# Performance work log

Hardware: AMD Instinct MI355X
Metric: run time of the kernel (lower is better)

The kernel has to match this reference:

```python
import jax, jax.numpy as jnp
import numpy as np

B, S, CACHE, HID, NH, NKV, HD, INTER = 2, 1024, 2048, 2048, 8, 1, 256, 16384
EPS = 1e-6
SOFTCAP = 50.0
SCALE = HD ** -0.5  # query_pre_attn_scalar is None -> head_dim**-0.5
NEG = -1e9


def _rms(x, w, eps=EPS):
    # Gemma RMSNorm: fp32 norm, output scaled by (1 + weight)
    x32 = x.astype(jnp.float32)
    n = x32 * jax.lax.rsqrt(jnp.mean(x32 * x32, axis=-1, keepdims=True) + eps)
    return (n * (1.0 + w)).astype(x.dtype)


def _rope(x, cos, sin):
    # half-split complex rotation (Gemma apply_rotary_emb): first half real, second half imag
    d2 = x.shape[-1] // 2
    x1, x2 = x[..., :d2], x[..., d2:]
    c = cos[None, :, None, :]
    s = sin[None, :, None, :]
    return jnp.concatenate([x1 * c - x2 * s, x1 * s + x2 * c], axis=-1).astype(x.dtype)


def setup_inputs() -> dict:
    key = jax.random.key(0)
    ks = jax.random.split(key, 8)
    sc = lambda k, sh, f: jax.random.normal(k, sh, jnp.float32) * f
    inp = {}
    inp["hidden_states"] = sc(ks[0], (B, S, HID), 1.0)
    inv = 1.0 / (10000.0 ** (np.arange(0, HD, 2, dtype=np.float32) / HD))
    t = np.arange(S, dtype=np.float32)[:, None] * inv[None, :]
    inp["cos"] = jnp.asarray(np.cos(t), jnp.float32)
    inp["sin"] = jnp.asarray(np.sin(t), jnp.float32)
    inp["kv_write_indices"] = jnp.arange(S, dtype=jnp.int32)
    inp["k_cache"] = jnp.zeros((B, CACHE, NKV, HD), jnp.float32)
    inp["v_cache"] = jnp.zeros((B, CACHE, NKV, HD), jnp.float32)
    i = jnp.arange(S)[:, None]
    j = jnp.arange(CACHE)[None, :]
    inp["mask"] = jnp.where(j <= i, 0.0, NEG).astype(jnp.float32)[None, None]  # [1,1,S,CACHE]
    inp["w_qkv"] = sc(ks[1], ((NH + 2 * NKV) * HD, HID), 0.02)
    inp["w_o"] = sc(ks[2], (HID, NH * HD), 0.02)
    inp["w_gate"] = sc(ks[3], (INTER, HID), 0.02)
    inp["w_up"] = sc(ks[4], (INTER, HID), 0.02)
    inp["w_down"] = sc(ks[5], (HID, INTER), 0.02)
    inp["ln_in"] = jnp.zeros((HID,), jnp.float32)
    inp["ln_post"] = jnp.zeros((HID,), jnp.float32)
    inp["q_norm"] = jnp.zeros((HD,), jnp.float32)
    inp["k_norm"] = jnp.zeros((HD,), jnp.float32)
    return inp


def reference(hidden_states, cos, sin, kv_write_indices, k_cache, v_cache, mask,
              w_qkv, w_o, w_gate, w_up, w_down, ln_in, ln_post, q_norm, k_norm):
    # ---- attention sub-block ----
    res = hidden_states
    x = _rms(hidden_states, ln_in)
    qkv = x @ w_qkv.T  # [B,S,(NH+2*NKV)*HD]
    xq, xk, xv = jnp.split(qkv, [NH * HD, NH * HD + NKV * HD], axis=-1)
    xq = xq.reshape(B, S, NH, HD)
    xk = xk.reshape(B, S, NKV, HD)
    xv = xv.reshape(B, S, NKV, HD)
    xq = _rms(xq, q_norm)  # QK-norm
    xk = _rms(xk, k_norm)
    xq = _rope(xq, cos, sin)
    xk = _rope(xk, cos, sin)
    # KV-cache write (index_copy_ on dim 1)
    k_cache = k_cache.at[:, kv_write_indices].set(xk)
    v_cache = v_cache.at[:, kv_write_indices].set(xv)
    key = jnp.repeat(k_cache, NH // NKV, axis=2)  # [B,CACHE,NH,HD]
    val = jnp.repeat(v_cache, NH // NKV, axis=2)
    scores = jnp.einsum('bshd,bthd->bhst', xq * SCALE, key)  # [B,NH,S,CACHE]
    scores = jnp.tanh(scores / SOFTCAP) * SOFTCAP            # logit softcapping
    probs = jax.nn.softmax(scores + mask, axis=-1)
    out = jnp.einsum('bhst,bthd->bshd', probs, val).reshape(B, S, NH * HD)
    h = res + out @ w_o.T
    # ---- MLP sub-block ----
    res = h
    x = _rms(h, ln_post)
    gate = jax.nn.gelu(x @ w_gate.T, approximate=True)
    up = x @ w_up.T
    return res + (gate * up) @ w_down.T
```

## Files before the change

### kernel.cpp

```cpp
#include <hip/hip_runtime.h>
#include <hip/hip_bf16.h>

typedef __attribute__((ext_vector_type(8))) short short8;
typedef __attribute__((ext_vector_type(4))) float f32x4;
typedef unsigned short u16;

#define B_N 2
#define S_N 1024
#define HID_N 2048
#define NH_N 8
#define HD_N 256
#define INTER_N 16384

#define GLB(p) ((const __attribute__((address_space(1))) void*)(p))
#define AS3(p) ((__attribute__((address_space(3))) void*)(p))

__device__ inline u16 f2b_rn(float f) {
    union { float f; unsigned int u; } x; x.f = f;
    unsigned int r = x.u + 0x7fffu + ((x.u >> 16) & 1u);
    return (u16)(r >> 16);
}
__device__ inline float b2f(u16 h) {
    union { unsigned int u; float f; } x; x.u = ((unsigned int)h) << 16;
    return x.f;
}
__device__ inline float gelu_fast(float v) {
    float z = 0.7978845608028654f * (v + 0.044715f * v * v * v);
    float e = exp2f(z * 2.8853900817779268f);
    float th = 1.f - 2.f * __builtin_amdgcn_rcpf(e + 1.f);
    return 0.5f * v * (1.f + th);
}

__global__ __launch_bounds__(256) void convert_f2b(const float* __restrict__ in,
                                                   u16* __restrict__ out, int n4) {
    int i = blockIdx.x * 256 + threadIdx.x;
    int stride = gridDim.x * 256;
    for (; i < n4; i += stride) {
        float4 v = reinterpret_cast<const float4*>(in)[i];
        u16 o[4] = { f2b_rn(v.x), f2b_rn(v.y), f2b_rn(v.z), f2b_rn(v.w) };
        reinterpret_cast<ulonglong1*>(out)[i] = *reinterpret_cast<ulonglong1*>(o);
    }
}

__global__ __launch_bounds__(256) void convert_gu(const float* __restrict__ wg,
                                                  const float* __restrict__ wu,
                                                  u16* __restrict__ out, int n4) {
    int i = blockIdx.x * 256 + threadIdx.x;
    int stride = gridDim.x * 256;
    for (; i < n4; i += stride) {
        const int e = i << 2;
        const int r = e >> 11, c = e & 2047;
        const int rg = ((r >> 5) << 6) + (r & 31);
        float4 g = reinterpret_cast<const float4*>(wg)[i];
        u16 og[4] = { f2b_rn(g.x), f2b_rn(g.y), f2b_rn(g.z), f2b_rn(g.w) };
        *reinterpret_cast<ulonglong1*>(out + (size_t)rg * 2048 + c) =
            *reinterpret_cast<ulonglong1*>(og);
        float4 u = reinterpret_cast<const float4*>(wu)[i];
        u16 ou[4] = { f2b_rn(u.x), f2b_rn(u.y), f2b_rn(u.z), f2b_rn(u.w) };
        *reinterpret_cast<ulonglong1*>(out + (size_t)(rg + 32) * 2048 + c) =
            *reinterpret_cast<ulonglong1*>(ou);
    }
}

__global__ __launch_bounds__(256) void rmsnorm_k(const float* __restrict__ x,
                                                 const float* __restrict__ w,
                                                 u16* __restrict__ out) {
    const int row = blockIdx.x;
    const int tid = threadIdx.x;
    const float* xr = x + (size_t)row * HID_N;
    const float4* xr4 = reinterpret_cast<const float4*>(xr);
    float4 a = xr4[tid * 2], b = xr4[tid * 2 + 1];
    float s = a.x*a.x + a.y*a.y + a.z*a.z + a.w*a.w
            + b.x*b.x + b.y*b.y + b.z*b.z + b.w*b.w;
    for (int off = 32; off > 0; off >>= 1) s += __shfl_xor(s, off, 64);
    __shared__ float red[4];
    if ((tid & 63) == 0) red[tid >> 6] = s;
    __syncthreads();
    float tot = red[0] + red[1] + red[2] + red[3];
    float inv = rsqrtf(tot * (1.0f / HID_N) + 1e-6f);
    const float4* w4 = reinterpret_cast<const float4*>(w);
    float4 wa = w4[tid * 2], wb = w4[tid * 2 + 1];
    short8 o;
    o[0] = (short)f2b_rn(a.x * inv * (1.f + wa.x));
    o[1] = (short)f2b_rn(a.y * inv * (1.f + wa.y));
    o[2] = (short)f2b_rn(a.z * inv * (1.f + wa.z));
    o[3] = (short)f2b_rn(a.w * inv * (1.f + wa.w));
    o[4] = (short)f2b_rn(b.x * inv * (1.f + wb.x));
    o[5] = (short)f2b_rn(b.y * inv * (1.f + wb.y));
    o[6] = (short)f2b_rn(b.z * inv * (1.f + wb.z));
    o[7] = (short)f2b_rn(b.w * inv * (1.f + wb.w));
    reinterpret_cast<short8*>(out + (size_t)row * HID_N)[tid] = o;
}

__global__ __launch_bounds__(256) void qkv_post_k(const float* __restrict__ qkv,
                                                  const float* __restrict__ cosb,
                                                  const float* __restrict__ sinb,
                                                  const int* __restrict__ kvw,
                                                  const float* __restrict__ qn,
                                                  const float* __restrict__ kn,
                                                  u16* __restrict__ qb,
                                                  u16* __restrict__ kb,
                                                  u16* __restrict__ vt) {
    const int bs = blockIdx.x, vi = blockIdx.y;
    const int b = bs >> 10, s = bs & 1023;
    const int tid = threadIdx.x;
    const float* row = qkv + (size_t)bs * 2560;
    const int sdst = kvw[s];
    if (vi == 9) {
        vt[((size_t)(b * 256 + tid)) * 1024 + sdst] = f2b_rn(row[2304 + tid]);
        return;
    }
    __shared__ float buf[256];
    __shared__ float red[4];
    float val = row[vi * 256 + tid];
    float ss = val * val;
    for (int off = 32; off > 0; off >>= 1) ss += __shfl_xor(ss, off, 64);
    if ((tid & 63) == 0) red[tid >> 6] = ss;
    __syncthreads();
    float ms = (red[0] + red[1] + red[2] + red[3]) * (1.f / 256.f) + 1e-6f;
    const float* nw = (vi < 8) ? qn : kn;
    float nrm = val * rsqrtf(ms) * (1.f + nw[tid]);
    buf[tid] = nrm;
    __syncthreads();
    const float cv = cosb[s * 128 + (tid & 127)];
    const float sv = sinb[s * 128 + (tid & 127)];
    float o;
    if (tid < 128) o = buf[tid] * cv - buf[tid + 128] * sv;
    else           o = buf[tid - 128] * sv + buf[tid] * cv;
    if (vi < 8) qb[(((size_t)(b * 8 + vi)) * 1024 + s) * 256 + tid] = f2b_rn(o * 0.0625f);
    else        kb[((size_t)(b * 1024 + sdst)) * 256 + tid] = f2b_rn(o);
}

__global__ __launch_bounds__(256) void attn_k(const u16* __restrict__ qb,
                                              const u16* __restrict__ kb,
                                              const u16* __restrict__ vt,
                                              float* __restrict__ po,
                                              float* __restrict__ pl) {
    const int qt = blockIdx.x;
    const int h  = blockIdx.y;
    const int c  = blockIdx.z >> 1;
    const int b  = blockIdx.z & 1;
    if (qt < 4 * c) return;
    const int tid = threadIdx.x, lane = tid & 63, wid = tid >> 6;
    const int g = lane >> 4, li = lane & 15;
    const int q0 = qt * 64 + wid * 16;
    const int kv_lo = c * 256;
    __shared__ u16 pbuf[4][16 * 32];

    short8 qf[8];
    const size_t qbase = (((size_t)(b * 8 + h)) * 1024 + q0 + li) * 256;
    #pragma unroll
    for (int kk = 0; kk < 8; ++kk)
        qf[kk] = *reinterpret_cast<const short8*>(qb + qbase + kk * 32 + g * 8);

    f32x4 o[16], o1;
    #pragma unroll
    for (int d = 0; d < 16; ++d) o[d] = f32x4{0.f, 0.f, 0.f, 0.f};
    o1 = f32x4{0.f, 0.f, 0.f, 0.f};
    short8 onesf;
    #pragma unroll
    for (int j = 0; j < 8; ++j) onesf[j] = (short)0x3F80;

    const int nt = (min(kv_lo + 256, q0 + 16) - kv_lo + 31) >> 5;
    const int prd = li * 32 + ((g * 8) ^ (((li >> 2) & 3) * 8));

    for (int t = 0; t < nt; ++t) {
        const int kv0 = kv_lo + t * 32;
        f32x4 sc[2];
        sc[0] = f32x4{0.f, 0.f, 0.f, 0.f};
        sc[1] = f32x4{0.f, 0.f, 0.f, 0.f};
        #pragma unroll
        for (int ch = 0; ch < 2; ++ch) {
            const size_t kbase = ((size_t)(b * 1024 + kv0 + ch * 16 + li)) * 256;
            #pragma unroll
            for (int kk = 0; kk < 8; ++kk) {
                short8 kf = *reinterpret_cast<const short8*>(kb + kbase + kk * 32 + g * 8);
                sc[ch] = __builtin_amdgcn_mfma_f32_16x16x32_bf16(qf[kk], kf, sc[ch], 0, 0, 0);
            }
        }
        #pragma unroll
        for (int reg = 0; reg < 4; ++reg) {
            const int qrow = q0 + g * 4 + reg;
            const int prow = g * 4 + reg;
            const int pswz = ((prow >> 2) & 3) * 8;
            #pragma unroll
            for (int ch = 0; ch < 2; ++ch) {
                const int col = kv0 + ch * 16 + li;
                float s = sc[ch][reg];
                float e = exp2f(s * 0.05770780163555854f);
                float th = 1.f - 2.f * __builtin_amdgcn_rcpf(e + 1.f);
                float pv = exp2f(th * 72.13475204444817f);
                pv = (col <= qrow) ? pv : 0.f;
                pbuf[wid][prow * 32 + ((ch * 16 + li) ^ pswz)] = f2b_rn(pv);
            }
        }
        short8 pf = *reinterpret_cast<const short8*>(&pbuf[wid][prd]);
        o1 = __builtin_amdgcn_mfma_f32_16x16x32_bf16(pf, onesf, o1, 0, 0, 0);
        #pragma unroll
        for (int dth = 0; dth < 2; ++dth) {
            short8 vf[8];
            #pragma unroll
            for (int d8 = 0; d8 < 8; ++d8) {
                const int dt = dth * 8 + d8;
                vf[d8] = *reinterpret_cast<const short8*>(
                    vt + ((size_t)(b * 256 + dt * 16 + li)) * 1024 + kv0 + g * 8);
            }
            #pragma unroll
            for (int d8 = 0; d8 < 8; ++d8)
                o[dth * 8 + d8] = __builtin_amdgcn_mfma_f32_16x16x32_bf16(pf, vf[d8], o[dth * 8 + d8], 0, 0, 0);
        }
    }
    const size_t pbase = ((size_t)((c * 2 + b) * 8 + h)) * 1024;
    #pragma unroll
    for (int reg = 0; reg < 4; ++reg) {
        const int row = q0 + g * 4 + reg;
        #pragma unroll
        for (int dt = 0; dt < 16; ++dt)
            po[(pbase + row) * 256 + dt * 16 + li] = o[dt][reg];
        if (li == 0) pl[pbase + row] = o1[reg];
    }
}

__global__ __launch_bounds__(256) void attn_red_k(const float* __restrict__ po,
                                                  const float* __restrict__ pl,
                                                  u16* __restrict__ out) {
    const int gid = blockIdx.x;
    const int b = gid >> 10, s = gid & 1023;
    const int tid = threadIdx.x;
    const int h = tid >> 5, d0 = (tid & 31) * 8;
    const int cmax = s >> 8;
    float l = 0.f;
    float4 a0 = float4{0.f, 0.f, 0.f, 0.f}, a1 = float4{0.f, 0.f, 0.f, 0.f};
    for (int ci = 0; ci <= cmax; ++ci) {
        const size_t r = ((size_t)((ci * 2 + b) * 8 + h)) * 1024 + s;
        l += pl[r];
        float4 b0 = *reinterpret_cast<const float4*>(po + r * 256 + d0);
        float4 b1 = *reinterpret_cast<const float4*>(po + r * 256 + d0 + 4);
        a0.x += b0.x; a0.y += b0.y; a0.z += b0.z; a0.w += b0.w;
        a1.x += b1.x; a1.y += b1.y; a1.z += b1.z; a1.w += b1.w;
    }
    const float inv = 1.f / l;
    u16 r[8] = { f2b_rn(a0.x * inv), f2b_rn(a0.y * inv), f2b_rn(a0.z * inv), f2b_rn(a0.w * inv),
                 f2b_rn(a1.x * inv), f2b_rn(a1.y * inv), f2b_rn(a1.z * inv), f2b_rn(a1.w * inv) };
    *reinterpret_cast<ulonglong2*>(out + ((size_t)gid) * 2048 + h * 256 + d0) =
        *reinterpret_cast<ulonglong2*>(r);
}

template <int EPI>
__global__ __launch_bounds__(256) void gemm_bt(const u16* __restrict__ A,
                                               const u16* __restrict__ W,
                                               const float* __restrict__ res,
                                               float* __restrict__ outf,
                                               int M, int N, int K) {
    __shared__ u16 As[2][128 * 64];
    __shared__ u16 Bs[2][128 * 64];
    const int tid = threadIdx.x, lane = tid & 63, wid = tid >> 6;
    const int g = lane >> 4, li = lane & 15;
    const int wr = wid >> 1, wc = wid & 1;
    const int m0 = blockIdx.x * 128, n0 = blockIdx.y * 128;

    f32x4 acc[4][4];
    #pragma unroll
    for (int m = 0; m < 4; ++m)
        #pragma unroll
        for (int n = 0; n < 4; ++n) acc[m][n] = f32x4{0.f, 0.f, 0.f, 0.f};

    const int lrow = lane >> 3;
    const int lcol = (lane & 7) ^ lrow;
    const u16* ga0 = A + (size_t)(m0 + wid * 32 + lrow) * K + lcol * 8;
    const u16* gb0 = W + (size_t)(n0 + wid * 32 + lrow) * K + lcol * 8;
    const int lbase = wid * 32 * 64;

    auto STAGE = [&](int buf, int k0) {
        #pragma unroll
        for (int i = 0; i < 4; ++i) {
            __builtin_amdgcn_global_load_lds(GLB(ga0 + k0 + (size_t)(i * 8) * K),
                                             AS3(&As[buf][lbase + i * 8 * 64]), 16, 0, 0);
            __builtin_amdgcn_global_load_lds(GLB(gb0 + k0 + (size_t)(i * 8) * K),
                                             AS3(&Bs[buf][lbase + i * 8 * 64]), 16, 0, 0);
        }
    };

    const int NT = K >> 6;
    STAGE(0, 0);
    int cur = 0;
    for (int t = 0; t < NT; ++t) {
        if (t + 1 < NT) {
            STAGE(cur ^ 1, (t + 1) << 6);
            asm volatile("s_waitcnt vmcnt(8)" ::: "memory");
        } else {
            asm volatile("s_waitcnt vmcnt(0)" ::: "memory");
        }
        __builtin_amdgcn_s_barrier();
        __builtin_amdgcn_sched_barrier(0);
        #pragma unroll
        for (int kh = 0; kh < 2; ++kh) {
            short8 af[4], bfr[4];
            #pragma unroll
            for (int m = 0; m < 4; ++m) {
                int rw = wr * 64 + m * 16 + li;
                int slot = (kh * 4 + g) ^ (rw & 7);
                af[m] = *reinterpret_cast<const short8*>(&As[cur][rw * 64 + slot * 8]);
            }
            #pragma unroll
            for (int n = 0; n < 4; ++n) {
                int rw = wc * 64 + n * 16 + li;
                int slot = (kh * 4 + g) ^ (rw & 7);
                bfr[n] = *reinterpret_cast<const short8*>(&Bs[cur][rw * 64 + slot * 8]);
            }
            #pragma unroll
            for (int m = 0; m < 4; ++m)
                #pragma unroll
                for (int n = 0; n < 4; ++n)
                    acc[m][n] = __builtin_amdgcn_mfma_f32_16x16x32_bf16(af[m], bfr[n], acc[m][n], 0, 0, 0);
        }
        __builtin_amdgcn_s_barrier();
        cur ^= 1;
    }

    #pragma unroll
    for (int m = 0; m < 4; ++m) {
        #pragma unroll
        for (int n = 0; n < 4; ++n) {
            #pragma unroll
            for (int reg = 0; reg < 4; ++reg) {
                int row = m0 + wr * 64 + m * 16 + g * 4 + reg;
                int col = n0 + wc * 64 + n * 16 + li;
                size_t idx = (size_t)row * N + col;
                float v = acc[m][n][reg];
                if (EPI == 0) outf[idx] = v;
                else          outf[idx] = v + res[idx];
            }
        }
    }
}

template <int EPI>
__global__ __launch_bounds__(1024) void gemm256(const u16* __restrict__ A,
                                                const u16* __restrict__ W,
                                                float* __restrict__ outf,
                                                u16* __restrict__ outb,
                                                int M, int N, int K, int kcN) {
    __shared__ u16 Als[2][256 * 64];
    __shared__ u16 Bls[2][256 * 64];
    const int tid = threadIdx.x, lane = tid & 63, wid = tid >> 6;
    const int g = lane >> 4, li = lane & 15;
    const int wm = wid >> 2, wn = wid & 3;
    const int m0 = blockIdx.y * 256, n0 = blockIdx.x * 256;

    int koff = 0, Keff = K;
    if (EPI == 4) {
        Keff = K / kcN;
        koff = blockIdx.z * Keff;
        outf += (size_t)blockIdx.z * M * N;
    }

    f32x4 acc[4][4];
    #pragma unroll
    for (int m = 0; m < 4; ++m)
        #pragma unroll
        for (int n = 0; n < 4; ++n) acc[m][n] = f32x4{0.f, 0.f, 0.f, 0.f};

    const int trow = tid >> 3;
    const int sgr = ((tid & 7) ^ (trow & 7)) * 8;
    const u16* Asrc = A + (size_t)(m0 + trow) * K + koff + sgr;
    const u16* Bsrc = W + (size_t)(n0 + trow) * K + koff + sgr;
    const int dstb = wid * 512;

    auto STAGE = [&](int bf, int kt) {
        const int k0 = kt << 6;
        #pragma unroll
        for (int i = 0; i < 2; ++i) {
            __builtin_amdgcn_global_load_lds(GLB(Asrc + (size_t)(i * 128) * K + k0),
                                             AS3(&Als[bf][i * 8192 + dstb]), 16, 0, 0);
            __builtin_amdgcn_global_load_lds(GLB(Bsrc + (size_t)(i * 128) * K + k0),
                                             AS3(&Bls[bf][i * 8192 + dstb]), 16, 0, 0);
        }
    };

    const int NT = Keff >> 6;
    STAGE(0, 0);
    int cur = 0;
    for (int t = 0; t < NT; ++t) {
        if (t + 1 < NT) {
            STAGE(cur ^ 1, t + 1);
            asm volatile("s_waitcnt vmcnt(4)" ::: "memory");
        } else {
            asm volatile("s_waitcnt vmcnt(0)" ::: "memory");
        }
        __builtin_amdgcn_s_barrier();
        __builtin_amdgcn_sched_barrier(0);
        #pragma unroll
        for (int kh = 0; kh < 2; ++kh) {
            short8 af[4], bfr[4];
            #pragma unroll
            for (int m = 0; m < 4; ++m) {
                const int rw = wm * 64 + m * 16 + li;
                const int slot = (kh * 4 + g) ^ (rw & 7);
                af[m] = *reinterpret_cast<const short8*>(&Als[cur][rw * 64 + slot * 8]);
            }
            #pragma unroll
            for (int n = 0; n < 4; ++n) {
                const int rw = wn * 64 + n * 16 + li;
                const int slot = (kh * 4 + g) ^ (rw & 7);
                bfr[n] = *reinterpret_cast<const short8*>(&Bls[cur][rw * 64 + slot * 8]);
            }
            #pragma unroll
            for (int m = 0; m < 4; ++m)
                #pragma unroll
                for (int n = 0; n < 4; ++n)
                    acc[m][n] = __builtin_amdgcn_mfma_f32_16x16x32_bf16(af[m], bfr[n], acc[m][n], 0, 0, 0);
        }
        __builtin_amdgcn_s_barrier();
        cur ^= 1;
    }

    if (EPI == 5) {
        #pragma unroll
        for (int m = 0; m < 4; ++m) {
            #pragma unroll
            for (int n = 0; n < 2; ++n) {
                const int col = (n0 >> 1) + wn * 32 + n * 16 + li;
                #pragma unroll
                for (int reg = 0; reg < 4; ++reg) {
                    const int row = m0 + wm * 64 + m * 16 + g * 4 + reg;
                    float gt = gelu_fast(acc[m][n][reg]);
                    float up = acc[m][n + 2][reg];
                    outb[(size_t)row * INTER_N + col] = f2b_rn(gt * up);
                }
            }
        }
    } else {
        #pragma unroll
        for (int m = 0; m < 4; ++m) {
            #pragma unroll
            for (int n = 0; n < 4; ++n) {
                #pragma unroll
                for (int reg = 0; reg < 4; ++reg) {
                    const int row = m0 + wm * 64 + m * 16 + g * 4 + reg;
                    const int col = n0 + wn * 64 + n * 16 + li;
                    outf[(size_t)row * N + col] = acc[m][n][reg];
                }
            }
        }
    }
}

__global__ __launch_bounds__(256) void reduce4_k(const float* __restrict__ part,
                                                 const float* __restrict__ res,
                                                 float* __restrict__ out, int n4) {
    int i = blockIdx.x * 256 + threadIdx.x;
    int stride = gridDim.x * 256;
    const size_t ps = (size_t)HID_N * B_N * S_N / 4;
    const float4* p4 = reinterpret_cast<const float4*>(part);
    const float4* r4 = reinterpret_cast<const float4*>(res);
    float4* o4 = reinterpret_cast<float4*>(out);
    for (; i < n4; i += stride) {
        float4 a = p4[i], b = p4[i + ps], c = p4[i + 2 * ps], d = p4[i + 3 * ps];
        float4 r = r4[i];
        float4 o;
        o.x = r.x + a.x + b.x + c.x + d.x;
        o.y = r.y + a.y + b.y + c.y + d.y;
        o.z = r.z + a.z + b.z + c.z + d.z;
        o.w = r.w + a.w + b.w + c.w + d.w;
        o4[i] = o;
    }
}

extern "C" void kernel_launch(void* const* d_in, const int* in_sizes, int n_in,
                              void* d_out, int out_size, void* d_ws, size_t ws_size,
                              hipStream_t stream) {
    (void)in_sizes; (void)n_in; (void)out_size; (void)ws_size;
    const float* hs     = (const float*)d_in[0];
    const float* cosb   = (const float*)d_in[1];
    const float* sinb   = (const float*)d_in[2];
    const int*   kvw    = (const int*)d_in[3];
    const float* wqkv   = (const float*)d_in[7];
    const float* wo     = (const float*)d_in[8];
    const float* wg     = (const float*)d_in[9];
    const float* wu     = (const float*)d_in[10];
    const float* wd     = (const float*)d_in[11];
    const float* ln_in  = (const float*)d_in[12];
    const float* ln_post= (const float*)d_in[13];
    const float* qn     = (const float*)d_in[14];
    const float* kn     = (const float*)d_in[15];
    float* out = (float*)d_out;

    char* p = (char*)d_ws;
    auto alloc = [&](size_t bytes) {
        char* r = p;
        p += (bytes + 255) & ~(size_t)255;
        return r;
    };
    u16* wqkv_b = (u16*)alloc(2560ull * 2048 * 2);
    u16* wo_b   = (u16*)alloc(2048ull * 2048 * 2);
    u16* wgu_b  = (u16*)alloc(32768ull * 2048 * 2);
    u16* wd_b   = (u16*)alloc(2048ull * 16384 * 2);
    u16* xn     = (u16*)alloc(2048ull * 2048 * 2);
    float* qkvf = (float*)alloc(2048ull * 2560 * 4);
    u16* qbuf   = (u16*)alloc(2ull * 8 * 1024 * 256 * 2);
    u16* kbuf   = (u16*)alloc(2ull * 1024 * 256 * 2);
    u16* vtbuf  = (u16*)alloc(2ull * 256 * 1024 * 2);
    u16* attn_o = (u16*)alloc(2048ull * 2048 * 2);
    float* hbuf = (float*)alloc(2048ull * 2048 * 4);
    u16* x2     = (u16*)alloc(2048ull * 2048 * 2);
    u16* actb   = (u16*)alloc(2048ull * 16384 * 2);
    float* po   = (float*)alloc(8ull * 8 * 1024 * 256 * 4);
    float* plse = (float*)alloc(8ull * 8 * 1024 * 4);
    float* partials = (float*)d_ws;

    auto conv = [&](const float* src, u16* dst, long n) {
        int n4 = (int)(n / 4);
        long blk = (n4 + 255) / 256;
        if (blk > 4096) blk = 4096;
        convert_f2b<<<dim3((unsigned)blk), dim3(256), 0, stream>>>(src, dst, n4);
    };
    conv(wqkv, wqkv_b, 2560l * 2048);
    conv(wo,   wo_b,   2048l * 2048);
    convert_gu<<<dim3(4096), dim3(256), 0, stream>>>(wg, wu, wgu_b, 8388608);
    conv(wd,   wd_b,   2048l * 16384);

    rmsnorm_k<<<dim3(2048), dim3(256), 0, stream>>>(hs, ln_in, xn);
    gemm_bt<0><<<dim3(16, 20), dim3(256), 0, stream>>>(xn, wqkv_b, nullptr,
                                                       qkvf, 2048, 2560, 2048);
    qkv_post_k<<<dim3(2048, 10), dim3(256), 0, stream>>>(qkvf, cosb, sinb, kvw, qn, kn,
                                                         qbuf, kbuf, vtbuf);
    attn_k<<<dim3(16, 8, 8), dim3(256), 0, stream>>>(qbuf, kbuf, vtbuf, po, plse);
    attn_red_k<<<dim3(2048), dim3(256), 0, stream>>>(po, plse, attn_o);
    gemm_bt<1><<<dim3(16, 16), dim3(256), 0, stream>>>(attn_o, wo_b, hs,
                                                       hbuf, 2048, 2048, 2048);
    rmsnorm_k<<<dim3(2048), dim3(256), 0, stream>>>(hbuf, ln_post, x2);
    gemm256<5><<<dim3(128, 8), dim3(1024), 0, stream>>>(x2, wgu_b, nullptr, actb,
                                                        2048, 16384, 2048, 1);
    gemm256<4><<<dim3(8, 8, 4), dim3(1024), 0, stream>>>(actb, wd_b, partials, nullptr,
                                                         2048, 2048, 16384, 4);
    reduce4_k<<<dim3(2048), dim3(256), 0, stream>>>(partials, hbuf, out, 1048576);
}
```

Measured before the change: 811.2 us.

## Replace GEMM kernels with unified 128x128 tile, 16-wave GEMM

Both the 4-wave 128x128 gemm_bt and the 16-wave 256x256 gemm256 are replaced by a single 16-wave kernel using 128x128 tiles, where each wave owns a 32x32 sub-tile. The gate/up weight interleave is changed from 32-row to 16-row groups to match the new per-wave column split. The aim is more waves per tile to hide latency and a larger grid for the big MLP GEMMs. In exchange, the arithmetic intensity per wave and the data reuse per tile drop, which raises LDS and global traffic per FLOP on the large GEMMs.

Measured after the change: 900.3 us. +11.0%, slower.

```diff
diff --git a/kernel.cpp b/kernel.cpp
--- a/kernel.cpp
+++ b/kernel.cpp
@@ -50,14 +50,14 @@
     for (; i < n4; i += stride) {
         const int e = i << 2;
         const int r = e >> 11, c = e & 2047;
-        const int rg = ((r >> 5) << 6) + (r & 31);
+        const int rg = ((r >> 4) << 5) + (r & 15);
         float4 g = reinterpret_cast<const float4*>(wg)[i];
         u16 og[4] = { f2b_rn(g.x), f2b_rn(g.y), f2b_rn(g.z), f2b_rn(g.w) };
         *reinterpret_cast<ulonglong1*>(out + (size_t)rg * 2048 + c) =
             *reinterpret_cast<ulonglong1*>(og);
         float4 u = reinterpret_cast<const float4*>(wu)[i];
         u16 ou[4] = { f2b_rn(u.x), f2b_rn(u.y), f2b_rn(u.z), f2b_rn(u.w) };
-        *reinterpret_cast<ulonglong1*>(out + (size_t)(rg + 32) * 2048 + c) =
+        *reinterpret_cast<ulonglong1*>(out + (size_t)(rg + 16) * 2048 + c) =
             *reinterpret_cast<ulonglong1*>(ou);
     }
 }
@@ -247,106 +247,18 @@
 }
 
 template <int EPI>
-__global__ __launch_bounds__(256) void gemm_bt(const u16* __restrict__ A,
-                                               const u16* __restrict__ W,
-                                               const float* __restrict__ res,
-                                               float* __restrict__ outf,
-                                               int M, int N, int K) {
-    __shared__ u16 As[2][128 * 64];
-    __shared__ u16 Bs[2][128 * 64];
-    const int tid = threadIdx.x, lane = tid & 63, wid = tid >> 6;
-    const int g = lane >> 4, li = lane & 15;
-    const int wr = wid >> 1, wc = wid & 1;
-    const int m0 = blockIdx.x * 128, n0 = blockIdx.y * 128;
-
-    f32x4 acc[4][4];
-    #pragma unroll
-    for (int m = 0; m < 4; ++m)
-        #pragma unroll
-        for (int n = 0; n < 4; ++n) acc[m][n] = f32x4{0.f, 0.f, 0.f, 0.f};
-
-    const int lrow = lane >> 3;
-    const int lcol = (lane & 7) ^ lrow;
-    const u16* ga0 = A + (size_t)(m0 + wid * 32 + lrow) * K + lcol * 8;
-    const u16* gb0 = W + (size_t)(n0 + wid * 32 + lrow) * K + lcol * 8;
-    const int lbase = wid * 32 * 64;
-
-    auto STAGE = [&](int buf, int k0) {
-        #pragma unroll
-        for (int i = 0; i < 4; ++i) {
-            __builtin_amdgcn_global_load_lds(GLB(ga0 + k0 + (size_t)(i * 8) * K),
-                                             AS3(&As[buf][lbase + i * 8 * 64]), 16, 0, 0);
-            __builtin_amdgcn_global_load_lds(GLB(gb0 + k0 + (size_t)(i * 8) * K),
-                                             AS3(&Bs[buf][lbase + i * 8 * 64]), 16, 0, 0);
-        }
-    };
-
-    const int NT = K >> 6;
-    STAGE(0, 0);
-    int cur = 0;
-    for (int t = 0; t < NT; ++t) {
-        if (t + 1 < NT) {
-            STAGE(cur ^ 1, (t + 1) << 6);
-            asm volatile("s_waitcnt vmcnt(8)" ::: "memory");
-        } else {
-            asm volatile("s_waitcnt vmcnt(0)" ::: "memory");
-        }
-        __builtin_amdgcn_s_barrier();
-        __builtin_amdgcn_sched_barrier(0);
-        #pragma unroll
-        for (int kh = 0; kh < 2; ++kh) {
-            short8 af[4], bfr[4];
-            #pragma unroll
-            for (int m = 0; m < 4; ++m) {
-                int rw = wr * 64 + m * 16 + li;
-                int slot = (kh * 4 + g) ^ (rw & 7);
-                af[m] = *reinterpret_cast<const short8*>(&As[cur][rw * 64 + slot * 8]);
-            }
-            #pragma unroll
-            for (int n = 0; n < 4; ++n) {
-                int rw = wc * 64 + n * 16 + li;
-                int slot = (kh * 4 + g) ^ (rw & 7);
-                bfr[n] = *reinterpret_cast<const short8*>(&Bs[cur][rw * 64 + slot * 8]);
-            }
-            #pragma unroll
-            for (int m = 0; m < 4; ++m)
-                #pragma unroll
-                for (int n = 0; n < 4; ++n)
-                    acc[m][n] = __builtin_amdgcn_mfma_f32_16x16x32_bf16(af[m], bfr[n], acc[m][n], 0, 0, 0);
-        }
-        __builtin_amdgcn_s_barrier();
-        cur ^= 1;
-    }
-
-    #pragma unroll
-    for (int m = 0; m < 4; ++m) {
-        #pragma unroll
-        for (int n = 0; n < 4; ++n) {
-            #pragma unroll
-            for (int reg = 0; reg < 4; ++reg) {
-                int row = m0 + wr * 64 + m * 16 + g * 4 + reg;
-                int col = n0 + wc * 64 + n * 16 + li;
-                size_t idx = (size_t)row * N + col;
-                float v = acc[m][n][reg];
-                if (EPI == 0) outf[idx] = v;
-                else          outf[idx] = v + res[idx];
-            }
-        }
-    }
-}
-
-template <int EPI>
-__global__ __launch_bounds__(1024) void gemm256(const u16* __restrict__ A,
-                                                const u16* __restrict__ W,
-                                                float* __restrict__ outf,
-                                                u16* __restrict__ outb,
-                                                int M, int N, int K, int kcN) {
-    __shared__ u16 Als[2][256 * 64];
-    __shared__ u16 Bls[2][256 * 64];
+__global__ __launch_bounds__(1024, 8) void gemm16w(const u16* __restrict__ A,
+                                                   const u16* __restrict__ W,
+                                                   const float* __restrict__ res,
+                                                   float* __restrict__ outf,
+                                                   u16* __restrict__ outb,
+                                                   int M, int N, int K, int kcN) {
+    __shared__ u16 Als[2][128 * 64];
+    __shared__ u16 Bls[2][128 * 64];
     const int tid = threadIdx.x, lane = tid & 63, wid = tid >> 6;
     const int g = lane >> 4, li = lane & 15;
     const int wm = wid >> 2, wn = wid & 3;
-    const int m0 = blockIdx.y * 256, n0 = blockIdx.x * 256;
+    const int m0 = blockIdx.y * 128, n0 = blockIdx.x * 128;
 
     int koff = 0, Keff = K;
     if (EPI == 4) {
@@ -355,11 +267,11 @@
         outf += (size_t)blockIdx.z * M * N;
     }
 
-    f32x4 acc[4][4];
+    f32x4 acc[2][2];
     #pragma unroll
-    for (int m = 0; m < 4; ++m)
-        #pragma unroll
-        for (int n = 0; n < 4; ++n) acc[m][n] = f32x4{0.f, 0.f, 0.f, 0.f};
+    for (int m = 0; m < 2; ++m)
+        #pragma unroll
+        for (int n = 0; n < 2; ++n) acc[m][n] = f32x4{0.f, 0.f, 0.f, 0.f};
 
     const int trow = tid >> 3;
     const int sgr = ((tid & 7) ^ (trow & 7)) * 8;
@@ -369,22 +281,21 @@
 
     auto STAGE = [&](int bf, int kt) {
         const int k0 = kt << 6;
-        #pragma unroll
-        for (int i = 0; i < 2; ++i) {
-            __builtin_amdgcn_global_load_lds(GLB(Asrc + (size_t)(i * 128) * K + k0),
-                                             AS3(&Als[bf][i * 8192 + dstb]), 16, 0, 0);
-            __builtin_amdgcn_global_load_lds(GLB(Bsrc + (size_t)(i * 128) * K + k0),
-                                             AS3(&Bls[bf][i * 8192 + dstb]), 16, 0, 0);
-        }
+        __builtin_amdgcn_global_load_lds(GLB(Asrc + k0), AS3(&Als[bf][dstb]), 16, 0, 0);
+        __builtin_amdgcn_global_load_lds(GLB(Bsrc + k0), AS3(&Bls[bf][dstb]), 16, 0, 0);
     };
 
     const int NT = Keff >> 6;
     STAGE(0, 0);
+    asm volatile("s_waitcnt vmcnt(0)" ::: "memory");
+    __builtin_amdgcn_s_barrier();
+    __builtin_amdgcn_sched_barrier(0);
+
     int cur = 0;
     for (int t = 0; t < NT; ++t) {
         if (t + 1 < NT) {
             STAGE(cur ^ 1, t + 1);
-            asm volatile("s_waitcnt vmcnt(4)" ::: "memory");
+            asm volatile("s_waitcnt vmcnt(2)" ::: "memory");
         } else {
             asm volatile("s_waitcnt vmcnt(0)" ::: "memory");
         }
@@ -392,23 +303,23 @@
         __builtin_amdgcn_sched_barrier(0);
         #pragma unroll
         for (int kh = 0; kh < 2; ++kh) {
-            short8 af[4], bfr[4];
-            #pragma unroll
-            for (int m = 0; m < 4; ++m) {
-                const int rw = wm * 64 + m * 16 + li;
+            short8 af[2], bfr[2];
+            #pragma unroll
+            for (int m = 0; m < 2; ++m) {
+                const int rw = wm * 32 + m * 16 + li;
                 const int slot = (kh * 4 + g) ^ (rw & 7);
                 af[m] = *reinterpret_cast<const short8*>(&Als[cur][rw * 64 + slot * 8]);
             }
             #pragma unroll
-            for (int n = 0; n < 4; ++n) {
-                const int rw = wn * 64 + n * 16 + li;
+            for (int n = 0; n < 2; ++n) {
+                const int rw = wn * 32 + n * 16 + li;
                 const int slot = (kh * 4 + g) ^ (rw & 7);
                 bfr[n] = *reinterpret_cast<const short8*>(&Bls[cur][rw * 64 + slot * 8]);
             }
             #pragma unroll
-            for (int m = 0; m < 4; ++m)
+            for (int m = 0; m < 2; ++m)
                 #pragma unroll
-                for (int n = 0; n < 4; ++n)
+                for (int n = 0; n < 2; ++n)
                     acc[m][n] = __builtin_amdgcn_mfma_f32_16x16x32_bf16(af[m], bfr[n], acc[m][n], 0, 0, 0);
         }
         __builtin_amdgcn_s_barrier();
@@ -417,29 +328,30 @@
 
     if (EPI == 5) {
         #pragma unroll
-        for (int m = 0; m < 4; ++m) {
+        for (int m = 0; m < 2; ++m) {
+            const int col = (n0 >> 1) + wn * 16 + li;
+            #pragma unroll
+            for (int reg = 0; reg < 4; ++reg) {
+                const int row = m0 + wm * 32 + m * 16 + g * 4 + reg;
+                float gt = gelu_fast(acc[m][0][reg]);
+                float up = acc[m][1][reg];
+                outb[(size_t)row * INTER_N + col] = f2b_rn(gt * up);
+            }
+        }
+    } else {
+        #pragma unroll
+        for (int m = 0; m < 2; ++m) {
             #pragma unroll
             for (int n = 0; n < 2; ++n) {
-                const int col = (n0 >> 1) + wn * 32 + n * 16 + li;
                 #pragma unroll
                 for (int reg = 0; reg < 4; ++reg) {
-                    const int row = m0 + wm * 64 + m * 16 + g * 4 + reg;
-                    float gt = gelu_fast(acc[m][n][reg]);
-                    float up = acc[m][n + 2][reg];
-                    outb[(size_t)row * INTER_N + col] = f2b_rn(gt * up);
-                }
-            }
-        }
-    } else {
-        #pragma unroll
-        for (int m = 0; m < 4; ++m) {
-            #pragma unroll
-            for (int n = 0; n < 4; ++n) {
-                #pragma unroll
-                for (int reg = 0; reg < 4; ++reg) {
-                    const int row = m0 + wm * 64 + m * 16 + g * 4 + reg;
-                    const int col = n0 + wn * 64 + n * 16 + li;
-                    outf[(size_t)row * N + col] = acc[m][n][reg];
+                    const int row = m0 + wm * 32 + m * 16 + g * 4 + reg;
+                    const int col = n0 + wn * 32 + n * 16 + li;
+                    size_t idx = (size_t)row * N + col;
+                    float v = acc[m][n][reg];
+                    if (EPI == 0)      outf[idx] = v;
+                    else if (EPI == 1) outf[idx] = v + res[idx];
+                    else               outf[idx] = v;
                 }
             }
         }
@@ -521,18 +433,18 @@
     conv(wd,   wd_b,   2048l * 16384);
 
     rmsnorm_k<<<dim3(2048), dim3(256), 0, stream>>>(hs, ln_in, xn);
-    gemm_bt<0><<<dim3(16, 20), dim3(256), 0, stream>>>(xn, wqkv_b, nullptr,
-                                                       qkvf, 2048, 2560, 2048);
+    gemm16w<0><<<dim3(20, 16), dim3(1024), 0, stream>>>(xn, wqkv_b, nullptr,
+                                                        qkvf, nullptr, 2048, 2560, 2048, 1);
     qkv_post_k<<<dim3(2048, 10), dim3(256), 0, stream>>>(qkvf, cosb, sinb, kvw, qn, kn,
                                                          qbuf, kbuf, vtbuf);
     attn_k<<<dim3(16, 8, 8), dim3(256), 0, stream>>>(qbuf, kbuf, vtbuf, po, plse);
     attn_red_k<<<dim3(2048), dim3(256), 0, stream>>>(po, plse, attn_o);
-    gemm_bt<1><<<dim3(16, 16), dim3(256), 0, stream>>>(attn_o, wo_b, hs,
-                                                       hbuf, 2048, 2048, 2048);
+    gemm16w<1><<<dim3(16, 16), dim3(1024), 0, stream>>>(attn_o, wo_b, hs,
+                                                        hbuf, nullptr, 2048, 2048, 2048, 1);
     rmsnorm_k<<<dim3(2048), dim3(256), 0, stream>>>(hbuf, ln_post, x2);
-    gemm256<5><<<dim3(128, 8), dim3(1024), 0, stream>>>(x2, wgu_b, nullptr, actb,
-                                                        2048, 16384, 2048, 1);
-    gemm256<4><<<dim3(8, 8, 4), dim3(1024), 0, stream>>>(actb, wd_b, partials, nullptr,
-                                                         2048, 2048, 16384, 4);
+    gemm16w<5><<<dim3(256, 16), dim3(1024), 0, stream>>>(x2, wgu_b, nullptr,
+                                                         nullptr, actb, 2048, 16384, 2048, 1);
+    gemm16w<4><<<dim3(16, 16, 4), dim3(1024), 0, stream>>>(actb, wd_b, nullptr,
+                                                           partials, nullptr, 2048, 2048, 16384, 4);
     reduce4_k<<<dim3(2048), dim3(256), 0, stream>>>(partials, hbuf, out, 1048576);
 }
```
